# Performance work log

Measured on AMD Instinct MI355X. Metric: run time of the kernel, lower is better.

## Reference

```python
import jax, jax.numpy as jnp
import numpy as np

D_MODEL = 1024
N_HEADS = 16
HEAD_DIM = D_MODEL // N_HEADS
BATCH = 2
SEQ = 2048


def setup_inputs() -> dict:
    key = jax.random.key(0)
    ks = jax.random.split(key, 9)
    s = 1.0 / np.sqrt(D_MODEL)
    x = jax.random.normal(ks[0], (BATCH, SEQ, D_MODEL), dtype=jnp.float32)
    # causal mask, broadcastable to (B, H, S, S); positions with 0 are masked out
    mask = jnp.tril(jnp.ones((SEQ, SEQ), dtype=bool))[None, None, :, :]
    Wq = jax.random.normal(ks[1], (D_MODEL, D_MODEL), dtype=jnp.float32) * s
    Wk = jax.random.normal(ks[2], (D_MODEL, D_MODEL), dtype=jnp.float32) * s
    Wv = jax.random.normal(ks[3], (D_MODEL, D_MODEL), dtype=jnp.float32) * s
    Wo = jax.random.normal(ks[4], (D_MODEL, D_MODEL), dtype=jnp.float32) * s
    bq = jnp.zeros((D_MODEL,), jnp.float32)
    bk = jnp.zeros((D_MODEL,), jnp.float32)
    bv = jnp.zeros((D_MODEL,), jnp.float32)
    bo = jnp.zeros((D_MODEL,), jnp.float32)
    return {"x": x, "mask": mask, "Wq": Wq, "bq": bq, "Wk": Wk, "bk": bk,
            "Wv": Wv, "bv": bv, "Wo": Wo, "bo": bo}


def reference(x, mask, Wq, bq, Wk, bk, Wv, bv, Wo, bo):
    B, S, _ = x.shape
    scale = HEAD_DIM ** -0.5
    # nn.Linear: y = x @ W.T + b ; W stored as (out, in)
    def proj(W, b):
        y = jnp.einsum('bsd,ed->bse', x, W) + b
        return y.reshape(B, S, N_HEADS, HEAD_DIM).transpose(0, 2, 1, 3)  # (B,H,S,Dh)
    q = proj(Wq, bq)
    k = proj(Wk, bk)
    v = proj(Wv, bv)
    scores = jnp.einsum('bhqd,bhkd->bhqk', q, k) * scale  # (B,H,S,S)
    scores = jnp.where(mask, scores, jnp.float32(-jnp.inf))
    weights = jax.nn.softmax(scores, axis=-1)
    attn = jnp.einsum('bhqk,bhkd->bhqd', weights, v)
    attn = attn.transpose(0, 2, 1, 3).reshape(B, S, D_MODEL)
    out = jnp.einsum('bsd,ed->bse', attn, Wo) + bo
    return out
```

## Files before the change

kernel.cpp:

```cpp
#include <hip/hip_runtime.h>
#include <hip/hip_bf16.h>

using bf16x8 = __attribute__((ext_vector_type(8))) short;
using f32x4  = __attribute__((ext_vector_type(4))) float;

#define SEQ      2048
#define DMODEL   1024
#define NHEADS   16
#define HDIM     64
#define MROWS    4096

__device__ __forceinline__ unsigned short f2bf(float f) {
  union { float f; unsigned u; } c; c.f = f;
  unsigned r = c.u + 0x7FFFu + ((c.u >> 16) & 1u);
  return (unsigned short)(r >> 16);
}

__device__ __forceinline__ unsigned cvtpk(float a, float b) {
  unsigned r;
  asm("v_cvt_pk_bf16_f32 %0, %1, %2" : "=v"(r) : "v"(a), "v"(b));
  return r;
}

__device__ __forceinline__ float fexp2(float x) {
  float r;
  asm("v_exp_f32 %0, %1" : "=v"(r) : "v"(x));
  return r;
}

__device__ __forceinline__ void gload16(const void* g, void* s) {
  __builtin_amdgcn_global_load_lds(
      (const __attribute__((address_space(1))) void*)g,
      (__attribute__((address_space(3))) void*)s, 16, 0, 0);
}

__global__ void cvt_all(const float* __restrict__ x,  const float* __restrict__ wq,
                        const float* __restrict__ wk, const float* __restrict__ wv,
                        const float* __restrict__ wo,
                        unsigned short* __restrict__ xb,  unsigned short* __restrict__ wqb,
                        unsigned short* __restrict__ wkb, unsigned short* __restrict__ wvb,
                        unsigned short* __restrict__ wob)
{
  int i = blockIdx.x * blockDim.x + threadIdx.x;
  const float* src; unsigned short* dst; int off;
  if (i < 1048576) { src = x; dst = xb; off = i; }
  else {
    int k = i - 1048576, seg = k >> 18; off = k & 262143;
    if      (seg == 0) { src = wq; dst = wqb; }
    else if (seg == 1) { src = wk; dst = wkb; }
    else if (seg == 2) { src = wv; dst = wvb; }
    else               { src = wo; dst = wob; }
  }
  const float4 v = ((const float4*)src)[off];
  ushort4 o;
  o.x = f2bf(v.x); o.y = f2bf(v.y); o.z = f2bf(v.z); o.w = f2bf(v.w);
  ((ushort4*)dst)[off] = o;
}

__global__ __launch_bounds__(256, 4)
void gemm_qkv(const unsigned short* __restrict__ Ab,
              const unsigned short* __restrict__ Wqb,
              const unsigned short* __restrict__ Wkb,
              const unsigned short* __restrict__ Wvb,
              const float* __restrict__ bq, const float* __restrict__ bk,
              const float* __restrict__ bv,
              unsigned short* __restrict__ Qo, unsigned short* __restrict__ Ko,
              unsigned short* __restrict__ Vto)
{
  __shared__ unsigned short As[128 * 64];
  __shared__ unsigned short Bs[128 * 64];
  const int t  = threadIdx.x;
  const int w  = t >> 6, l = t & 63;
  const int lr = l & 15, lg = l >> 4;
  const int bm = blockIdx.x / 24;
  const int bn = blockIdx.x % 24;
  const int which = bn >> 3;
  const unsigned short* Bsrc = which == 0 ? Wqb : (which == 1 ? Wkb : Wvb);
  const float* biasp = which == 0 ? bq : (which == 1 ? bk : bv);
  const int bnw = bn & 7;
  const int wm = w >> 1, wn = w & 1;

  const char* Agp = (const char*)Ab + (size_t)bm * 128 * 2048;
  const char* Bgp = (const char*)Bsrc + (size_t)bnw * 128 * 2048;

  f32x4 acc[4][4];
  #pragma unroll
  for (int a = 0; a < 4; ++a)
    #pragma unroll
    for (int b = 0; b < 4; ++b) acc[a][b] = (f32x4){0.f, 0.f, 0.f, 0.f};

  for (int kt = 0; kt < 16; ++kt) {
    const int kbyte = kt * 128;
    #pragma unroll
    for (int i = 0; i < 4; ++i) {
      int idx  = i * 256 + t;
      int row  = idx >> 3;
      int colb = (idx & 7) << 4;
      int scol = colb ^ ((row & 7) << 4);
      gload16(Agp + (size_t)row * 2048 + kbyte + scol, (char*)As + idx * 16);
      gload16(Bgp + (size_t)row * 2048 + kbyte + scol, (char*)Bs + idx * 16);
    }
    __syncthreads();
    #pragma unroll
    for (int kk = 0; kk < 2; ++kk) {
      bf16x8 af[4], bfr[4];
      #pragma unroll
      for (int x = 0; x < 4; ++x) {
        int ra = wm * 64 + x * 16 + lr;
        int rb = wn * 64 + x * 16 + lr;
        int cb = (kk * 64 + lg * 16) ^ ((lr & 7) << 4);
        af[x]  = *(const bf16x8*)((const char*)As + ra * 128 + cb);
        bfr[x] = *(const bf16x8*)((const char*)Bs + rb * 128 + cb);
      }
      #pragma unroll
      for (int xa = 0; xa < 4; ++xa)
        #pragma unroll
        for (int xb = 0; xb < 4; ++xb)
          acc[xa][xb] = __builtin_amdgcn_mfma_f32_16x16x32_bf16(af[xa], bfr[xb], acc[xa][xb], 0, 0, 0);
    }
    __syncthreads();
  }

  #pragma unroll
  for (int xb = 0; xb < 4; ++xb) {
    int colg = bnw * 128 + wn * 64 + xb * 16 + lr;
    int h  = colg >> 6, dh = colg & 63;
    float biasv = biasp[colg];
    #pragma unroll
    for (int xa = 0; xa < 4; ++xa) {
      int row0 = bm * 128 + wm * 64 + xa * 16 + lg * 4;
      #pragma unroll
      for (int i = 0; i < 4; ++i) {
        int m = row0 + i;
        int b = m >> 11, s = m & 2047;
        float v = acc[xa][xb][i] + biasv;
        if (which == 0) {
          Qo[(((size_t)(b * NHEADS + h)) * SEQ + s) * HDIM + dh] = f2bf(v * 0.180336881f);
        } else if (which == 1) {
          Ko[(((size_t)(b * NHEADS + h)) * SEQ + s) * HDIM + dh] = f2bf(v);
        } else {
          Vto[(((size_t)(b * NHEADS + h)) * HDIM + dh) * SEQ + s] = f2bf(v);
        }
      }
    }
  }
}

__device__ __forceinline__ void stage_kv64(const char* Kg, const char* Vg,
                                           char* Kl, char* Vl, int nb, int t)
{
  #pragma unroll
  for (int i = 0; i < 2; ++i) {
    int idx = i * 256 + t;
    int row = idx >> 3, colb = (idx & 7) << 4;
    int scol = colb ^ ((row & 7) << 4);
    gload16(Kg + (size_t)(nb + row) * 128 + scol, Kl + idx * 16);
    gload16(Vg + (size_t)row * 4096 + (size_t)nb * 2 + scol, Vl + idx * 16);
  }
}

__device__ __forceinline__ void attn_sub16(const char* Kl, const char* Vl, char* Pw,
                                           const bf16x8 (&qf)[2], const bf16x8 ones,
                                           f32x4 (&o)[4], f32x4 &accL,
                                           int q0w, int kbase, bool diag, int lr, int lg)
{
  bf16x8 kf[4][2];
  #pragma unroll
  for (int n = 0; n < 4; ++n)
    #pragma unroll
    for (int kk = 0; kk < 2; ++kk)
      kf[n][kk] = *(const bf16x8*)(Kl + (size_t)(n * 16 + lr) * 128 +
                                   ((kk * 64 + lg * 16) ^ ((lr & 7) << 4)));
  f32x4 st[4];
  __builtin_amdgcn_s_setprio(1);
  #pragma unroll
  for (int n = 0; n < 4; ++n) {
    f32x4 acc = (f32x4){0.f, 0.f, 0.f, 0.f};
    #pragma unroll
    for (int kk = 0; kk < 2; ++kk)
      acc = __builtin_amdgcn_mfma_f32_16x16x32_bf16(kf[n][kk], qf[kk], acc, 0, 0, 0);
    st[n] = acc;
  }
  __builtin_amdgcn_s_setprio(0);
  if (diag) {
    #pragma unroll
    for (int n = 0; n < 4; ++n) {
      #pragma unroll
      for (int i = 0; i < 4; ++i) {
        int key = kbase + n * 16 + lg * 4 + i;
        if (key > q0w + lr) st[n][i] = -3.0e38f;
      }
    }
  }
  #pragma unroll
  for (int n = 0; n < 4; ++n) {
    float p0 = fexp2(st[n][0]);
    float p1 = fexp2(st[n][1]);
    float p2 = fexp2(st[n][2]);
    float p3 = fexp2(st[n][3]);
    uint2 pw;
    pw.x = cvtpk(p0, p1);
    pw.y = cvtpk(p2, p3);
    *(uint2*)(Pw + lr * 128 + ((n * 32 + lg * 8) ^ ((lr & 7) << 4))) = pw;
  }
  __builtin_amdgcn_s_setprio(1);
  #pragma unroll
  for (int kk = 0; kk < 2; ++kk) {
    bf16x8 af = *(const bf16x8*)(Pw + lr * 128 + ((kk * 64 + lg * 16) ^ ((lr & 7) << 4)));
    accL = __builtin_amdgcn_mfma_f32_16x16x32_bf16(af, ones, accL, 0, 0, 0);
    #pragma unroll
    for (int n = 0; n < 4; ++n) {
      bf16x8 vf = *(const bf16x8*)(Vl + (size_t)(n * 16 + lr) * 128 +
                    ((kk * 64 + lg * 16) ^ ((lr & 7) << 4)));
      o[n] = __builtin_amdgcn_mfma_f32_16x16x32_bf16(af, vf, o[n], 0, 0, 0);
    }
  }
  __builtin_amdgcn_s_setprio(0);
}

__global__ __launch_bounds__(256, 2)
void attn_fwd(const unsigned short* __restrict__ Q,
              const unsigned short* __restrict__ K,
              const unsigned short* __restrict__ Vt,
              unsigned short* __restrict__ O)
{
  const int t = threadIdx.x;
  const int w = t >> 6, l = t & 63;
  const int lr = l & 15, lg = l >> 4;
  const int bh = blockIdx.x & 31;
  const int p  = blockIdx.x >> 5;
  const int qtA = p, qtB = 31 - p;
  const int b = bh >> 4, h = bh & 15;
  const int q0wA = qtA * 64 + w * 16;
  const int q0wB = qtB * 64 + w * 16;

  const unsigned short* Qp = Q + (size_t)bh * SEQ * HDIM;
  const char* Kg = (const char*)(K  + (size_t)bh * SEQ * HDIM);
  const char* Vg = (const char*)(Vt + (size_t)bh * HDIM * SEQ);

  __shared__ unsigned short Klds[2][64 * 64];
  __shared__ unsigned short Vlds[2][64 * 64];
  __shared__ unsigned short Plds[4][16][64];
  char* Pw = (char*)Plds[w];

  bf16x8 qfA[2], qfB[2];
  #pragma unroll
  for (int kk = 0; kk < 2; ++kk) {
    qfA[kk] = *(const bf16x8*)(Qp + (size_t)(q0wA + lr) * HDIM + kk * 32 + lg * 8);
    qfB[kk] = *(const bf16x8*)(Qp + (size_t)(q0wB + lr) * HDIM + kk * 32 + lg * 8);
  }

  bf16x8 ones;
  #pragma unroll
  for (int e = 0; e < 8; ++e) ones[e] = (short)0x3F80;

  f32x4 oA[4], oB[4];
  f32x4 accLA = (f32x4){0.f, 0.f, 0.f, 0.f};
  f32x4 accLB = (f32x4){0.f, 0.f, 0.f, 0.f};
  #pragma unroll
  for (int n = 0; n < 4; ++n) {
    oA[n] = (f32x4){0.f, 0.f, 0.f, 0.f};
    oB[n] = (f32x4){0.f, 0.f, 0.f, 0.f};
  }

  stage_kv64(Kg, Vg, (char*)Klds[0], (char*)Vlds[0], 0, t);
  {
    int kb1 = (1 <= qtA) ? 1 : 0;
    stage_kv64(Kg, Vg, (char*)Klds[1], (char*)Vlds[1], kb1 * 64, t);
  }

  int cur = 0;
  for (int j = 0; j < 33; ++j) {
    if (j < 32)
      asm volatile("s_waitcnt vmcnt(4)" ::: "memory");
    else
      asm volatile("s_waitcnt vmcnt(0)" ::: "memory");
    __builtin_amdgcn_s_barrier();
    asm volatile("" ::: "memory");
    if (j <= qtA) {
      attn_sub16((const char*)Klds[cur], (const char*)Vlds[cur], Pw, qfA, ones,
                 oA, accLA, q0wA, j * 64, j == qtA, lr, lg);
    } else {
      int kb = j - qtA - 1;
      attn_sub16((const char*)Klds[cur], (const char*)Vlds[cur], Pw, qfB, ones,
                 oB, accLB, q0wB, kb * 64, j == 32, lr, lg);
    }
    asm volatile("" ::: "memory");
    __builtin_amdgcn_s_barrier();
    asm volatile("" ::: "memory");
    if (j + 2 < 33) {
      int jn = j + 2;
      int kbn = (jn <= qtA) ? jn : jn - qtA - 1;
      stage_kv64(Kg, Vg, (char*)Klds[cur], (char*)Vlds[cur], kbn * 64, t);
    }
    cur ^= 1;
  }

  #pragma unroll
  for (int n = 0; n < 4; ++n) {
    int col = h * HDIM + n * 16 + lr;
    #pragma unroll
    for (int i = 0; i < 4; ++i) {
      int srowA = q0wA + lg * 4 + i;
      int srowB = q0wB + lg * 4 + i;
      O[((size_t)(b * SEQ + srowA)) * DMODEL + col] = f2bf(oA[n][i] / accLA[i]);
      O[((size_t)(b * SEQ + srowB)) * DMODEL + col] = f2bf(oB[n][i] / accLB[i]);
    }
  }
}

__global__ __launch_bounds__(256, 2)
void gemm_out(const unsigned short* __restrict__ Ab, const unsigned short* __restrict__ Bb,
              const float* __restrict__ bias, float* __restrict__ C)
{
  __shared__ unsigned short As[128 * 64];
  __shared__ unsigned short Bs[64 * 64];
  const int t  = threadIdx.x;
  const int w  = t >> 6, l = t & 63;
  const int lr = l & 15, lg = l >> 4;
  const int bm = blockIdx.x >> 4;
  const int bn = blockIdx.x & 15;
  const int wm = w >> 1, wn = w & 1;

  const char* Agp = (const char*)Ab + (size_t)bm * 128 * 2048;
  const char* Bgp = (const char*)Bb + (size_t)bn * 64 * 2048;

  f32x4 acc[4][2];
  #pragma unroll
  for (int a = 0; a < 4; ++a)
    #pragma unroll
    for (int b = 0; b < 2; ++b) acc[a][b] = (f32x4){0.f, 0.f, 0.f, 0.f};

  for (int kt = 0; kt < 16; ++kt) {
    const int kbyte = kt * 128;
    #pragma unroll
    for (int i = 0; i < 4; ++i) {
      int idx  = i * 256 + t;
      int row  = idx >> 3;
      int colb = (idx & 7) << 4;
      int scol = colb ^ ((row & 7) << 4);
      gload16(Agp + (size_t)row * 2048 + kbyte + scol, (char*)As + idx * 16);
    }
    #pragma unroll
    for (int i = 0; i < 2; ++i) {
      int idx  = i * 256 + t;
      int row  = idx >> 3;
      int colb = (idx & 7) << 4;
      int scol = colb ^ ((row & 7) << 4);
      gload16(Bgp + (size_t)row * 2048 + kbyte + scol, (char*)Bs + idx * 16);
    }
    __syncthreads();
    #pragma unroll
    for (int kk = 0; kk < 2; ++kk) {
      bf16x8 af[4], bfr[2];
      #pragma unroll
      for (int x = 0; x < 4; ++x) {
        int ra = wm * 64 + x * 16 + lr;
        int cb = (kk * 64 + lg * 16) ^ ((lr & 7) << 4);
        af[x]  = *(const bf16x8*)((const char*)As + ra * 128 + cb);
      }
      #pragma unroll
      for (int x = 0; x < 2; ++x) {
        int rb = wn * 32 + x * 16 + lr;
        int cb = (kk * 64 + lg * 16) ^ ((lr & 7) << 4);
        bfr[x] = *(const bf16x8*)((const char*)Bs + rb * 128 + cb);
      }
      #pragma unroll
      for (int xa = 0; xa < 4; ++xa)
        #pragma unroll
        for (int xb = 0; xb < 2; ++xb)
          acc[xa][xb] = __builtin_amdgcn_mfma_f32_16x16x32_bf16(af[xa], bfr[xb], acc[xa][xb], 0, 0, 0);
    }
    __syncthreads();
  }
  #pragma unroll
  for (int xb = 0; xb < 2; ++xb) {
    int col = bn * 64 + wn * 32 + xb * 16 + lr;
    float bvv = bias[col];
    #pragma unroll
    for (int xa = 0; xa < 4; ++xa) {
      int row0 = bm * 128 + wm * 64 + xa * 16 + lg * 4;
      #pragma unroll
      for (int i = 0; i < 4; ++i)
        C[(size_t)(row0 + i) * DMODEL + col] = acc[xa][xb][i] + bvv;
    }
  }
}

extern "C" void kernel_launch(void* const* d_in, const int* in_sizes, int n_in,
                              void* d_out, int out_size, void* d_ws, size_t ws_size,
                              hipStream_t stream)
{
  const float* x  = (const float*)d_in[0];
  const float* Wq = (const float*)d_in[2];
  const float* bq = (const float*)d_in[3];
  const float* Wk = (const float*)d_in[4];
  const float* bk = (const float*)d_in[5];
  const float* Wv = (const float*)d_in[6];
  const float* bv = (const float*)d_in[7];
  const float* Wo = (const float*)d_in[8];
  const float* bo = (const float*)d_in[9];

  char* ws = (char*)d_ws;
  const size_t MB = 1024 * 1024;
  unsigned short* xb   = (unsigned short*)(ws + 0);
  unsigned short* Wqb  = (unsigned short*)(ws + 8  * MB);
  unsigned short* Wkb  = (unsigned short*)(ws + 10 * MB);
  unsigned short* Wvb  = (unsigned short*)(ws + 12 * MB);
  unsigned short* Wob  = (unsigned short*)(ws + 14 * MB);
  unsigned short* Qb   = (unsigned short*)(ws + 16 * MB);
  unsigned short* Kb   = (unsigned short*)(ws + 24 * MB);
  unsigned short* Vtb  = (unsigned short*)(ws + 32 * MB);
  unsigned short* Attn = (unsigned short*)(ws + 40 * MB);

  cvt_all<<<8192, 256, 0, stream>>>(x, Wq, Wk, Wv, Wo, xb, Wqb, Wkb, Wvb, Wob);
  gemm_qkv<<<768, 256, 0, stream>>>(xb, Wqb, Wkb, Wvb, bq, bk, bv, Qb, Kb, Vtb);
  attn_fwd<<<512, 256, 0, stream>>>(Qb, Kb, Vtb, Attn);
  gemm_out<<<512, 256, 0, stream>>>(Attn, Wob, bo, (float*)d_out);
}
```

Measured before the change: 99.92 us.

## Software-pipeline attention loop: overlap QK/softmax of tile j with PV of tile j-1

Splits the per-tile attention body into a QK+exp part and a PV part and skews them so each iteration runs PV for the previous key tile and QK for the current one. The P scratch buffer is double-buffered per wave, and K and V staging is decoupled so V is fetched one tile later than K, with adjusted vmcnt waits and a final epilogue PV step. The aim is more independent MFMA and exp work per iteration so the dependency from QK through exp to PV stalls less. In exchange it uses more LDS and a more complex wait-count schedule, which could go wrong at tile boundaries.

New measurement: 99.70 us. About the same (-0.2%).

```diff
diff --git a/kernel.cpp b/kernel.cpp
--- a/kernel.cpp
+++ b/kernel.cpp
@@ -146,8 +146,7 @@
   }
 }
 
-__device__ __forceinline__ void stage_kv64(const char* Kg, const char* Vg,
-                                           char* Kl, char* Vl, int nb, int t)
+__device__ __forceinline__ void stage_k64(const char* Kg, char* Kl, int nb, int t)
 {
   #pragma unroll
   for (int i = 0; i < 2; ++i) {
@@ -155,14 +154,22 @@
     int row = idx >> 3, colb = (idx & 7) << 4;
     int scol = colb ^ ((row & 7) << 4);
     gload16(Kg + (size_t)(nb + row) * 128 + scol, Kl + idx * 16);
+  }
+}
+__device__ __forceinline__ void stage_v64(const char* Vg, char* Vl, int nb, int t)
+{
+  #pragma unroll
+  for (int i = 0; i < 2; ++i) {
+    int idx = i * 256 + t;
+    int row = idx >> 3, colb = (idx & 7) << 4;
+    int scol = colb ^ ((row & 7) << 4);
     gload16(Vg + (size_t)row * 4096 + (size_t)nb * 2 + scol, Vl + idx * 16);
   }
 }
 
-__device__ __forceinline__ void attn_sub16(const char* Kl, const char* Vl, char* Pw,
-                                           const bf16x8 (&qf)[2], const bf16x8 ones,
-                                           f32x4 (&o)[4], f32x4 &accL,
-                                           int q0w, int kbase, bool diag, int lr, int lg)
+__device__ __forceinline__ void qk_part(const char* Kl, char* Pc,
+                                        const bf16x8 (&qf)[2],
+                                        int q0w, int kbase, bool diag, int lr, int lg)
 {
   bf16x8 kf[4][2];
   #pragma unroll
@@ -184,13 +191,12 @@
   __builtin_amdgcn_s_setprio(0);
   if (diag) {
     #pragma unroll
-    for (int n = 0; n < 4; ++n) {
+    for (int n = 0; n < 4; ++n)
       #pragma unroll
       for (int i = 0; i < 4; ++i) {
         int key = kbase + n * 16 + lg * 4 + i;
         if (key > q0w + lr) st[n][i] = -3.0e38f;
       }
-    }
   }
   #pragma unroll
   for (int n = 0; n < 4; ++n) {
@@ -201,12 +207,18 @@
     uint2 pw;
     pw.x = cvtpk(p0, p1);
     pw.y = cvtpk(p2, p3);
-    *(uint2*)(Pw + lr * 128 + ((n * 32 + lg * 8) ^ ((lr & 7) << 4))) = pw;
-  }
+    *(uint2*)(Pc + lr * 128 + ((n * 32 + lg * 8) ^ ((lr & 7) << 4))) = pw;
+  }
+}
+
+__device__ __forceinline__ void pv_part(const char* Vl, const char* Pc,
+                                        const bf16x8 ones,
+                                        f32x4 (&o)[4], f32x4 &accL, int lr, int lg)
+{
   __builtin_amdgcn_s_setprio(1);
   #pragma unroll
   for (int kk = 0; kk < 2; ++kk) {
-    bf16x8 af = *(const bf16x8*)(Pw + lr * 128 + ((kk * 64 + lg * 16) ^ ((lr & 7) << 4)));
+    bf16x8 af = *(const bf16x8*)(Pc + lr * 128 + ((kk * 64 + lg * 16) ^ ((lr & 7) << 4)));
     accL = __builtin_amdgcn_mfma_f32_16x16x32_bf16(af, ones, accL, 0, 0, 0);
     #pragma unroll
     for (int n = 0; n < 4; ++n) {
@@ -240,7 +252,7 @@
 
   __shared__ unsigned short Klds[2][64 * 64];
   __shared__ unsigned short Vlds[2][64 * 64];
-  __shared__ unsigned short Plds[4][16][64];
+  __shared__ unsigned short Plds[4][2][16][64];
   char* Pw = (char*)Plds[w];
 
   bf16x8 qfA[2], qfB[2];
@@ -263,38 +275,49 @@
     oB[n] = (f32x4){0.f, 0.f, 0.f, 0.f};
   }
 
-  stage_kv64(Kg, Vg, (char*)Klds[0], (char*)Vlds[0], 0, t);
-  {
-    int kb1 = (1 <= qtA) ? 1 : 0;
-    stage_kv64(Kg, Vg, (char*)Klds[1], (char*)Vlds[1], kb1 * 64, t);
-  }
-
-  int cur = 0;
+  stage_k64(Kg, (char*)Klds[0], 0, t);
+  { int nb1 = (1 <= qtA) ? 64 : 0;
+    stage_k64(Kg, (char*)Klds[1], nb1, t); }
+  stage_v64(Vg, (char*)Vlds[0], 0, t);
+
   for (int j = 0; j < 33; ++j) {
     if (j < 32)
       asm volatile("s_waitcnt vmcnt(4)" ::: "memory");
     else
-      asm volatile("s_waitcnt vmcnt(0)" ::: "memory");
+      asm volatile("s_waitcnt vmcnt(2)" ::: "memory");
     __builtin_amdgcn_s_barrier();
     asm volatile("" ::: "memory");
-    if (j <= qtA) {
-      attn_sub16((const char*)Klds[cur], (const char*)Vlds[cur], Pw, qfA, ones,
-                 oA, accLA, q0wA, j * 64, j == qtA, lr, lg);
-    } else {
-      int kb = j - qtA - 1;
-      attn_sub16((const char*)Klds[cur], (const char*)Vlds[cur], Pw, qfB, ones,
-                 oB, accLB, q0wB, kb * 64, j == 32, lr, lg);
+    if (j >= 1) {
+      const char* Vp = (const char*)Vlds[(j - 1) & 1];
+      const char* Pp = Pw + ((j - 1) & 1) * 2048;
+      if (j - 1 <= qtA) pv_part(Vp, Pp, ones, oA, accLA, lr, lg);
+      else              pv_part(Vp, Pp, ones, oB, accLB, lr, lg);
+    }
+    {
+      const char* Kp2 = (const char*)Klds[j & 1];
+      char* Pc = Pw + (j & 1) * 2048;
+      if (j <= qtA) qk_part(Kp2, Pc, qfA, q0wA, j * 64, j == qtA, lr, lg);
+      else          qk_part(Kp2, Pc, qfB, q0wB, (j - qtA - 1) * 64, j == 32, lr, lg);
     }
     asm volatile("" ::: "memory");
     __builtin_amdgcn_s_barrier();
     asm volatile("" ::: "memory");
-    if (j + 2 < 33) {
+    if (j + 2 <= 32) {
       int jn = j + 2;
-      int kbn = (jn <= qtA) ? jn : jn - qtA - 1;
-      stage_kv64(Kg, Vg, (char*)Klds[cur], (char*)Vlds[cur], kbn * 64, t);
-    }
-    cur ^= 1;
-  }
+      int nb = ((jn <= qtA) ? jn : jn - qtA - 1) * 64;
+      stage_k64(Kg, (char*)Klds[j & 1], nb, t);
+    }
+    if (j + 1 <= 32) {
+      int jn = j + 1;
+      int nb = ((jn <= qtA) ? jn : jn - qtA - 1) * 64;
+      stage_v64(Vg, (char*)Vlds[jn & 1], nb, t);
+    }
+  }
+
+  asm volatile("s_waitcnt vmcnt(0)" ::: "memory");
+  __builtin_amdgcn_s_barrier();
+  asm volatile("" ::: "memory");
+  pv_part((const char*)Vlds[0], Pw, ones, oB, accLB, lr, lg);
 
   #pragma unroll
   for (int n = 0; n < 4; ++n) {
```
